# Kernel tuning notes

Measured on AMD Instinct MI355X. Metric: run time of the kernel, lower is better.

The kernel has to match this reference:

```python
import jax, jax.numpy as jnp
import numpy as np

EPS = 1e-07
NEG_DIAG = -10.0
HDCE_GAMMA = 1.0

def l2_normalize(x):
    # norm = (sum(x^2, axis=1))^(1/2); out = x / (norm + 1e-7)
    norm = jnp.sqrt(jnp.sum(x * x, axis=1, keepdims=True))
    return x / (norm + EPS)

def setup_inputs() -> dict:
    key = jax.random.key(0)
    k1, k2, k3 = jax.random.split(key, 3)
    N, D, DG = 4096, 256, 256
    feat_q = jax.random.normal(k1, (N, D), dtype=jnp.float32)
    feat_k = jax.random.normal(k2, (N, D), dtype=jnp.float32)
    feat_g = jax.random.normal(k3, (N, DG), dtype=jnp.float32)
    return {"feat_q": feat_q, "feat_k": feat_k, "feat_g": feat_g}

def reference(feat_q, feat_k, feat_g):
    N = feat_q.shape[0]
    fq = l2_normalize(feat_q)  # computed in original but unused for weight_out
    fk = l2_normalize(feat_k)
    fg = l2_normalize(feat_g)
    # batched self-similarity with batch_dim_for_bmm = 1 -> [1, N, N]
    spatial_k = jnp.einsum('nd,md->nm', fk, fk)[None]
    spatial_g = jnp.einsum('nd,md->nm', fg, fg)[None]
    spatial_kg = (spatial_k + 1.0 + EPS) / (spatial_g + 1.0 + EPS)
    diag = jnp.eye(N, dtype=bool)[None]  # [1, N, N]
    weight_seed = jnp.where(diag, NEG_DIAG, spatial_kg)
    weight_out = jax.nn.softmax(weight_seed / HDCE_GAMMA, axis=2)
    wmax = jnp.max(weight_out, axis=2, keepdims=True)
    return weight_out / wmax
```

## Files before the change

### kernel.cpp

```cpp
#include <hip/hip_runtime.h>
#include <hip/hip_bf16.h>
#include <cmath>

typedef __attribute__((ext_vector_type(8))) short short8;
typedef __attribute__((ext_vector_type(4))) float f32x4;

#define EPS_F 1e-7f
#define NEG_DIAG_F -10.0f
#define NPART 128

__device__ __forceinline__ void gload_lds16(const void* gptr, void* ldsptr) {
    __builtin_amdgcn_global_load_lds(
        (const __attribute__((address_space(1))) unsigned int*)gptr,
        (__attribute__((address_space(3))) unsigned int*)ldsptr,
        16, 0, 0);
}

__global__ void norm_cast_kernel(const float* __restrict__ fk, const float* __restrict__ fg,
                                 __hip_bfloat16* __restrict__ fkb, __hip_bfloat16* __restrict__ fgb,
                                 float* __restrict__ P, int N, int D) {
    int n = blockIdx.x;
    int t = threadIdx.x;
    float xk = fk[(size_t)n * D + t];
    float xg = fg[(size_t)n * D + t];
    float sk = xk * xk, sg = xg * xg;
#pragma unroll
    for (int off = 32; off > 0; off >>= 1) {
        sk += __shfl_xor(sk, off, 64);
        sg += __shfl_xor(sg, off, 64);
    }
    __shared__ float lsk[4], lsg[4];
    int w = t >> 6, l = t & 63;
    if (l == 0) { lsk[w] = sk; lsg[w] = sg; }
    __syncthreads();
    sk = lsk[0] + lsk[1] + lsk[2] + lsk[3];
    sg = lsg[0] + lsg[1] + lsg[2] + lsg[3];
    float rkv = 1.0f / (sqrtf(sk) + EPS_F);
    float rgv = 1.0f / (sqrtf(sg) + EPS_F);
    fkb[(size_t)n * D + t] = __float2bfloat16(xk * rkv);
    fgb[(size_t)n * D + t] = __float2bfloat16(xg * rgv);
    if (t < NPART) P[(size_t)n * NPART + t] = 0.0f;
}

__global__ __launch_bounds__(256, 5) void gram64_kernel(
    const __hip_bfloat16* __restrict__ fkb, const __hip_bfloat16* __restrict__ fgb,
    float* __restrict__ out, float* __restrict__ P, int N, int D) {

    __shared__ __align__(16) char smem[17408 + 512];
    float* bnc = (float*)smem;
    int* lmax = (int*)(smem + 17408);

    int bx = blockIdx.x, by = blockIdx.y;
    if (bx < by) return;
    int r0 = by * 64, c0 = bx * 64;

    int t = threadIdx.x;
    int w = t >> 6, l = t & 63;
    int wr = w >> 1, wc = w & 1;
    int lr = l & 15, lg = l >> 4;

    if (t < NPART) lmax[t] = 0;

    int aoff[2], boff[2];
#pragma unroll
    for (int m = 0; m < 2; ++m) {
        int row = wr * 32 + m * 16 + lr;
        aoff[m] = row * 64 + ((lg ^ ((row >> 1) & 3)) << 4);
    }
#pragma unroll
    for (int n = 0; n < 2; ++n) {
        int row = wc * 32 + n * 16 + lr;
        boff[n] = row * 64 + ((lg ^ ((row >> 1) & 3)) << 4);
    }

    int srow = t >> 2;
    int scsw = ((t & 3) ^ ((srow >> 1) & 3)) << 4;
    const size_t rowbytes = (size_t)D * 2;
    size_t gA = (size_t)(r0 + srow) * rowbytes + scsw;
    size_t gB = (size_t)(c0 + srow) * rowbytes + scsw;
    int sdst = (t >> 6) << 10;

    f32x4 acck[2][2], accg[2][2];
    f32x4 zero = {0.f, 0.f, 0.f, 0.f};
#pragma unroll
    for (int m = 0; m < 2; ++m)
#pragma unroll
        for (int n = 0; n < 2; ++n) { acck[m][n] = zero; accg[m][n] = zero; }

    for (int k0 = 0; k0 < D; k0 += 32) {
        size_t kb = (size_t)k0 * 2;
        gload_lds16((const char*)fkb + gA + kb, smem + sdst);
        gload_lds16((const char*)fgb + gA + kb, smem + 4096 + sdst);
        gload_lds16((const char*)fkb + gB + kb, smem + 8192 + sdst);
        gload_lds16((const char*)fgb + gB + kb, smem + 12288 + sdst);
        __syncthreads();

        short8 ak[2], ag[2], bk[2], bg[2];
#pragma unroll
        for (int m = 0; m < 2; ++m) {
            ak[m] = *(const short8*)(smem + aoff[m]);
            ag[m] = *(const short8*)(smem + 4096 + aoff[m]);
        }
#pragma unroll
        for (int n = 0; n < 2; ++n) {
            bk[n] = *(const short8*)(smem + 8192 + boff[n]);
            bg[n] = *(const short8*)(smem + 12288 + boff[n]);
        }
        __builtin_amdgcn_s_setprio(1);
#pragma unroll
        for (int m = 0; m < 2; ++m)
#pragma unroll
            for (int n = 0; n < 2; ++n) {
                acck[m][n] = __builtin_amdgcn_mfma_f32_16x16x32_bf16(ak[m], bk[n], acck[m][n], 0, 0, 0);
                accg[m][n] = __builtin_amdgcn_mfma_f32_16x16x32_bf16(ag[m], bg[n], accg[m][n], 0, 0, 0);
            }
        __builtin_amdgcn_s_setprio(0);
        __syncthreads();
    }

#pragma unroll
    for (int m = 0; m < 2; ++m)
#pragma unroll
        for (int j = 0; j < 4; ++j) {
            int lrow = wr * 32 + m * 16 + lg * 4 + j;
#pragma unroll
            for (int n = 0; n < 2; ++n) {
                float dk = acck[m][n][j];
                float dg = accg[m][n][j];
                float s = (dk + 1.0f + EPS_F) * __builtin_amdgcn_rcpf(dg + 1.0f + EPS_F);
                if (r0 + lrow == c0 + wc * 32 + n * 16 + lr) s = NEG_DIAG_F;
                acck[m][n][j] = s;
            }
        }

#pragma unroll
    for (int m = 0; m < 2; ++m)
#pragma unroll
        for (int j = 0; j < 4; ++j) {
            float pm = fmaxf(acck[m][0][j], acck[m][1][j]);
#pragma unroll
            for (int off = 1; off < 16; off <<= 1)
                pm = fmaxf(pm, __shfl_xor(pm, off, 64));
            if (lr == 0) atomicMax(&lmax[wr * 32 + m * 16 + lg * 4 + j], __float_as_int(pm));
        }
#pragma unroll
    for (int n = 0; n < 2; ++n) {
        float cm = acck[0][n][0];
#pragma unroll
        for (int m = 0; m < 2; ++m)
#pragma unroll
            for (int j = 0; j < 4; ++j) cm = fmaxf(cm, acck[m][n][j]);
        cm = fmaxf(cm, __shfl_xor(cm, 16, 64));
        cm = fmaxf(cm, __shfl_xor(cm, 32, 64));
        if (lg == 0) atomicMax(&lmax[64 + wc * 32 + n * 16 + lr], __float_as_int(cm));
    }

#pragma unroll
    for (int m = 0; m < 2; ++m)
#pragma unroll
        for (int n = 0; n < 2; ++n)
#pragma unroll
            for (int j = 0; j < 4; ++j)
                bnc[(wr * 32 + m * 16 + lg * 4 + j) * 68 + wc * 32 + n * 16 + lr] = acck[m][n][j];
    __syncthreads();

#pragma unroll
    for (int i = 0; i < 4; ++i) {
        int rr = i * 16 + (t >> 4);
        f32x4 v = *(const f32x4*)&bnc[rr * 68 + (t & 15) * 4];
        *(f32x4*)(out + (size_t)(r0 + rr) * N + c0 + (t & 15) * 4) = v;
    }
    if (t < 64) {
        P[(size_t)(r0 + t) * NPART + bx] = __int_as_float(lmax[t]);
    } else if (t < 128 && bx > by) {
        P[(size_t)(c0 + t - 64) * NPART + 64 + by] = __int_as_float(lmax[t]);
    }

    if (bx > by) {
        __syncthreads();
#pragma unroll
        for (int m = 0; m < 2; ++m)
#pragma unroll
            for (int n = 0; n < 2; ++n)
#pragma unroll
                for (int j = 0; j < 4; ++j)
                    bnc[(wc * 32 + n * 16 + lr) * 68 + wr * 32 + m * 16 + lg * 4 + j] = acck[m][n][j];
        __syncthreads();
#pragma unroll
        for (int i = 0; i < 4; ++i) {
            int rr = i * 16 + (t >> 4);
            f32x4 v = *(const f32x4*)&bnc[rr * 68 + (t & 15) * 4];
            *(f32x4*)(out + (size_t)(c0 + rr) * N + r0 + (t & 15) * 4) = v;
        }
    }
}

__global__ void finalize_kernel(float* __restrict__ out, const float* __restrict__ P, int N) {
    int row = blockIdx.x;
    int t = threadIdx.x;
    int j = t & 63;
    float m = fmaxf(P[(size_t)row * NPART + j], P[(size_t)row * NPART + 64 + j]);
#pragma unroll
    for (int off = 1; off < 64; off <<= 1)
        m = fmaxf(m, __shfl_xor(m, off, 64));
    float4* o4 = (float4*)(out + (size_t)row * N);
    int n4 = N >> 2;
    for (int i = t; i < n4; i += 256) {
        float4 v = o4[i];
        v.x = __expf(v.x - m);
        v.y = __expf(v.y - m);
        v.z = __expf(v.z - m);
        v.w = __expf(v.w - m);
        o4[i] = v;
    }
}

extern "C" void kernel_launch(void* const* d_in, const int* in_sizes, int n_in,
                              void* d_out, int out_size, void* d_ws, size_t ws_size,
                              hipStream_t stream) {
    const float* fk = (const float*)d_in[1];
    const float* fg = (const float*)d_in[2];
    float* out = (float*)d_out;

    int N = (int)llround(sqrt((double)out_size));
    int D = in_sizes[1] / N;

    char* ws = (char*)d_ws;
    float* P = (float*)ws;
    __hip_bfloat16* fkb = (__hip_bfloat16*)(ws + (size_t)N * NPART * 4);
    __hip_bfloat16* fgb = (__hip_bfloat16*)(ws + (size_t)N * NPART * 4 + (size_t)N * D * 2);

    norm_cast_kernel<<<N, D, 0, stream>>>(fk, fg, fkb, fgb, P, N, D);

    gram64_kernel<<<dim3(N / 64, N / 64), 256, 0, stream>>>(fkb, fgb, out, P, N, D);

    finalize_kernel<<<N, 256, 0, stream>>>(out, P, N);
}
```

Baseline: 68.64 us.

## Double-buffer LDS tiles in gram kernel to overlap global loads with MFMA

Splits shared memory into two 16KB stages. The next K-slice's global-to-LDS loads are issued before computing on the current one, using explicit vmcnt waits and raw barriers instead of __syncthreads on every step. The K loop is hardcoded to D=256 (8 steps of 32, 512-byte rows), and occupancy drops from 5 to 4 blocks because of the larger LDS footprint. The transpose staging stride also changes from 68 to 66 floats to alter bank mapping. With that stride, 16-byte LDS vector reads are no longer 16-byte aligned.

```diff
diff --git a/kernel.cpp b/kernel.cpp
--- a/kernel.cpp
+++ b/kernel.cpp
@@ -42,13 +42,13 @@
     if (t < NPART) P[(size_t)n * NPART + t] = 0.0f;
 }
 
-__global__ __launch_bounds__(256, 5) void gram64_kernel(
+__global__ __launch_bounds__(256, 4) void gram64_kernel(
     const __hip_bfloat16* __restrict__ fkb, const __hip_bfloat16* __restrict__ fgb,
     float* __restrict__ out, float* __restrict__ P, int N, int D) {
 
-    __shared__ __align__(16) char smem[17408 + 512];
+    __shared__ __align__(16) char smem[33280];
     float* bnc = (float*)smem;
-    int* lmax = (int*)(smem + 17408);
+    int* lmax = (int*)(smem + 32768);
 
     int bx = blockIdx.x, by = blockIdx.y;
     if (bx < by) return;
@@ -75,10 +75,11 @@
 
     int srow = t >> 2;
     int scsw = ((t & 3) ^ ((srow >> 1) & 3)) << 4;
-    const size_t rowbytes = (size_t)D * 2;
-    size_t gA = (size_t)(r0 + srow) * rowbytes + scsw;
-    size_t gB = (size_t)(c0 + srow) * rowbytes + scsw;
-    int sdst = (t >> 6) << 10;
+    const char* pAk = (const char*)fkb + (size_t)(r0 + srow) * 512 + scsw;
+    const char* pAg = (const char*)fgb + (size_t)(r0 + srow) * 512 + scsw;
+    const char* pBk = (const char*)fkb + (size_t)(c0 + srow) * 512 + scsw;
+    const char* pBg = (const char*)fgb + (size_t)(c0 + srow) * 512 + scsw;
+    int sdst = w << 10;
 
     f32x4 acck[2][2], accg[2][2];
     f32x4 zero = {0.f, 0.f, 0.f, 0.f};
@@ -87,35 +88,54 @@
 #pragma unroll
         for (int n = 0; n < 2; ++n) { acck[m][n] = zero; accg[m][n] = zero; }
 
-    for (int k0 = 0; k0 < D; k0 += 32) {
-        size_t kb = (size_t)k0 * 2;
-        gload_lds16((const char*)fkb + gA + kb, smem + sdst);
-        gload_lds16((const char*)fgb + gA + kb, smem + 4096 + sdst);
-        gload_lds16((const char*)fkb + gB + kb, smem + 8192 + sdst);
-        gload_lds16((const char*)fgb + gB + kb, smem + 12288 + sdst);
-        __syncthreads();
-
-        short8 ak[2], ag[2], bk[2], bg[2];
-#pragma unroll
-        for (int m = 0; m < 2; ++m) {
-            ak[m] = *(const short8*)(smem + aoff[m]);
-            ag[m] = *(const short8*)(smem + 4096 + aoff[m]);
-        }
-#pragma unroll
-        for (int n = 0; n < 2; ++n) {
-            bk[n] = *(const short8*)(smem + 8192 + boff[n]);
-            bg[n] = *(const short8*)(smem + 12288 + boff[n]);
-        }
+    gload_lds16(pAk, smem + sdst);
+    gload_lds16(pAg, smem + 4096 + sdst);
+    gload_lds16(pBk, smem + 8192 + sdst);
+    gload_lds16(pBg, smem + 12288 + sdst);
+
+    for (int ks = 0; ks < 8; ++ks) {
+        char* cur = smem + (ks & 1) * 16384;
+        if (ks < 7) {
+            char* nxt = smem + (((ks & 1) ^ 1)) * 16384;
+            int kb = (ks + 1) * 64;
+            gload_lds16(pAk + kb, nxt + sdst);
+            gload_lds16(pAg + kb, nxt + 4096 + sdst);
+            gload_lds16(pBk + kb, nxt + 8192 + sdst);
+            gload_lds16(pBg + kb, nxt + 12288 + sdst);
+            asm volatile("s_waitcnt vmcnt(4)" ::: "memory");
+        } else {
+            asm volatile("s_waitcnt vmcnt(0)" ::: "memory");
+        }
+        __builtin_amdgcn_s_barrier();
+        __builtin_amdgcn_sched_barrier(0);
+
+        short8 ak[2], bk[2];
+#pragma unroll
+        for (int m = 0; m < 2; ++m) ak[m] = *(const short8*)(cur + aoff[m]);
+#pragma unroll
+        for (int n = 0; n < 2; ++n) bk[n] = *(const short8*)(cur + 8192 + boff[n]);
         __builtin_amdgcn_s_setprio(1);
 #pragma unroll
         for (int m = 0; m < 2; ++m)
 #pragma unroll
-            for (int n = 0; n < 2; ++n) {
+            for (int n = 0; n < 2; ++n)
                 acck[m][n] = __builtin_amdgcn_mfma_f32_16x16x32_bf16(ak[m], bk[n], acck[m][n], 0, 0, 0);
+        __builtin_amdgcn_s_setprio(0);
+
+        short8 ag[2], bg[2];
+#pragma unroll
+        for (int m = 0; m < 2; ++m) ag[m] = *(const short8*)(cur + 4096 + aoff[m]);
+#pragma unroll
+        for (int n = 0; n < 2; ++n) bg[n] = *(const short8*)(cur + 12288 + boff[n]);
+        __builtin_amdgcn_s_setprio(1);
+#pragma unroll
+        for (int m = 0; m < 2; ++m)
+#pragma unroll
+            for (int n = 0; n < 2; ++n)
                 accg[m][n] = __builtin_amdgcn_mfma_f32_16x16x32_bf16(ag[m], bg[n], accg[m][n], 0, 0, 0);
-            }
         __builtin_amdgcn_s_setprio(0);
-        __syncthreads();
+        __builtin_amdgcn_sched_barrier(0);
+        __builtin_amdgcn_s_barrier();
     }
 
 #pragma unroll
@@ -161,13 +181,13 @@
         for (int n = 0; n < 2; ++n)
 #pragma unroll
             for (int j = 0; j < 4; ++j)
-                bnc[(wr * 32 + m * 16 + lg * 4 + j) * 68 + wc * 32 + n * 16 + lr] = acck[m][n][j];
+                bnc[(wr * 32 + m * 16 + lg * 4 + j) * 66 + wc * 32 + n * 16 + lr] = acck[m][n][j];
     __syncthreads();
 
 #pragma unroll
     for (int i = 0; i < 4; ++i) {
         int rr = i * 16 + (t >> 4);
-        f32x4 v = *(const f32x4*)&bnc[rr * 68 + (t & 15) * 4];
+        f32x4 v = *(const f32x4*)&bnc[rr * 66 + (t & 15) * 4];
         *(f32x4*)(out + (size_t)(r0 + rr) * N + c0 + (t & 15) * 4) = v;
     }
     if (t < 64) {
@@ -184,12 +204,12 @@
             for (int n = 0; n < 2; ++n)
 #pragma unroll
                 for (int j = 0; j < 4; ++j)
-                    bnc[(wc * 32 + n * 16 + lr) * 68 + wr * 32 + m * 16 + lg * 4 + j] = acck[m][n][j];
+                    bnc[(wc * 32 + n * 16 + lr) * 66 + wr * 32 + m * 16 + lg * 4 + j] = acck[m][n][j];
         __syncthreads();
 #pragma unroll
         for (int i = 0; i < 4; ++i) {
             int rr = i * 16 + (t >> 4);
-            f32x4 v = *(const f32x4*)&bnc[rr * 68 + (t & 15) * 4];
+            f32x4 v = *(const f32x4*)&bnc[rr * 66 + (t & 15) * 4];
             *(f32x4*)(out + (size_t)(c0 + rr) * N + r0 + (t & 15) * 4) = v;
         }
     }
```

After: 71.34 us. +3.9%, slower.
